# Optimization experiments

Hardware: AMD Instinct MI355X
Metric: run time of the kernel (lower is better)

The kernel has to match this reference:

```python
import jax, jax.numpy as jnp
import numpy as np

# skimage color deconvolution constants: hed_from_rgb = inv(rgb_from_hed)
_RGB_FROM_HED = np.array([[0.65, 0.70, 0.29],
                          [0.07, 0.99, 0.11],
                          [0.27, 0.57, 0.78]], dtype=np.float64)
_HED_FROM_RGB = np.linalg.inv(_RGB_FROM_HED).astype(np.float32)
_LOG_ADJUST = float(np.log(1e-6))  # skimage separate_stains log base


def setup_inputs() -> dict:
    key = jax.random.key(0)
    k1, = jax.random.split(key, 1)
    x = jax.random.uniform(k1, (64, 3, 512, 512), dtype=jnp.float32)  # RGB patches in [0,1]
    gamma = jnp.ones((1,), dtype=jnp.float32)   # InstanceNorm2d affine weight
    beta = jnp.zeros((1,), dtype=jnp.float32)   # InstanceNorm2d affine bias
    return {"x": x, "gamma": gamma, "beta": beta}


def reference(x, gamma, beta):
    h_weights = jnp.asarray(_HED_FROM_RGB[:, 0])  # only H (hematoxylin) column needed, shape (3,)

    # --- skimage.color.separate_stains, batched (replaces per-sample CPU loop) ---
    rgb = jnp.clip(x, 0.0, 1.0)                  # torch.clamp(t, 0, 1)
    rgb = jnp.maximum(rgb, 1e-6)                 # avoid log(0)
    od = jnp.log(rgb) / _LOG_ADJUST              # optical density, (B,3,H,W)
    h = jnp.einsum('bchw,c->bhw', od, h_weights) # stain matrix multiply, H channel only
    h = jnp.maximum(h, 0.0)[:, None, :, :]       # (B,1,H,W), skimage clips stains at 0

    # --- FFT magnitude spectrum ---
    fft = jnp.fft.fft2(h, norm='forward')        # complex64, scaled by 1/(H*W)
    fft = jnp.fft.fftshift(fft, axes=(-2, -1))
    mag = jnp.abs(fft)

    # --- _normalize_log_fft: log1p then per-image min-max ---
    log_mag = jnp.log1p(mag)
    mn = jnp.min(log_mag, axis=(-2, -1), keepdims=True)
    mx = jnp.max(log_mag, axis=(-2, -1), keepdims=True)
    rng = mx - mn
    safe_rng = jnp.where(rng > 0, rng, 1.0)
    normed = jnp.where(rng > 0, (log_mag - mn) / safe_rng, 0.0)

    # --- nn.InstanceNorm2d(1, affine=True), eps=1e-5 ---
    mu = jnp.mean(normed, axis=(-2, -1), keepdims=True)
    var = jnp.var(normed, axis=(-2, -1), keepdims=True)
    out = (normed - mu) * jax.lax.rsqrt(var + 1e-5)
    return out * gamma[None, :, None, None] + beta[None, :, None, None]
```

## Files before the change

### kernel.cpp

```cpp
#include <hip/hip_runtime.h>
#include <hip/hip_fp16.h>
#include <math.h>


#define PI_F 3.14159265358979323846f
#define FROW 264
#define LMSTR 264
#define LVMAX 1.6f
#define QE (65535.0f / LVMAX)
#define QD (LVMAX / 65535.0f)
#define XSTR 568

__device__ __forceinline__ int MU(int p) {
    return ((p >> 6) * 72) + (p & 56) + ((p & 7) ^ ((p >> 3) & 7));
}
__device__ __forceinline__ int odrev(int k) {
    return ((k & 7) << 6) | (k & 56) | (k >> 6);
}

__device__ __forceinline__ float2 cadd(float2 a, float2 b) { return make_float2(a.x + b.x, a.y + b.y); }
__device__ __forceinline__ float2 csub(float2 a, float2 b) { return make_float2(a.x - b.x, a.y - b.y); }
__device__ __forceinline__ float2 cmul(float2 a, float2 w) {
    return make_float2(a.x * w.x - a.y * w.y, a.x * w.y + a.y * w.x);
}

__device__ __forceinline__ void dft8(float2 v[8]) {
    const float s = 0.70710678118654752f;
    float2 a0 = cadd(v[0], v[4]), b0 = csub(v[0], v[4]);
    float2 a1 = cadd(v[1], v[5]), b1 = csub(v[1], v[5]);
    float2 a2 = cadd(v[2], v[6]), b2 = csub(v[2], v[6]);
    float2 a3 = cadd(v[3], v[7]), b3 = csub(v[3], v[7]);
    b1 = make_float2(s * (b1.x + b1.y), s * (b1.y - b1.x));
    b2 = make_float2(b2.y, -b2.x);
    b3 = make_float2(s * (b3.y - b3.x), -s * (b3.x + b3.y));
    float2 c0 = cadd(a0, a2), c1 = cadd(a1, a3);
    float2 d0 = csub(a0, a2), d1 = csub(a1, a3);
    d1 = make_float2(d1.y, -d1.x);
    v[0] = cadd(c0, c1); v[4] = csub(c0, c1);
    v[2] = cadd(d0, d1); v[6] = csub(d0, d1);
    float2 e0 = cadd(b0, b2), e1 = cadd(b1, b3);
    float2 f0 = csub(b0, b2), f1 = csub(b1, b3);
    f1 = make_float2(f1.y, -f1.x);
    v[1] = cadd(e0, e1); v[5] = csub(e0, e1);
    v[3] = cadd(f0, f1); v[7] = csub(f0, f1);
}

__device__ __forceinline__ void fft512_reg(float2* Xw, const float2* TW, int lane) {
    float2 v[8];
    #pragma unroll
    for (int m = 0; m < 8; ++m) v[m] = Xw[MU(lane + (m << 6))];
    dft8(v);
    #pragma unroll
    for (int m = 1; m < 8; ++m) v[m] = cmul(v[m], TW[(lane * m) & 511]);
    #pragma unroll
    for (int m = 0; m < 8; ++m) Xw[MU((m << 6) + lane)] = v[m];
    __builtin_amdgcn_wave_barrier();
    const int b = lane >> 3, t = lane & 7;
    const int base2 = (b << 6) + t;
    #pragma unroll
    for (int m = 0; m < 8; ++m) v[m] = Xw[MU(base2 + (m << 3))];
    dft8(v);
    #pragma unroll
    for (int m = 1; m < 8; ++m) v[m] = cmul(v[m], TW[(t * m) << 3]);
    #pragma unroll
    for (int m = 0; m < 8; ++m) Xw[MU(base2 + (m << 3))] = v[m];
    __builtin_amdgcn_wave_barrier();
    const int base3 = (b << 6) + (t << 3);
    #pragma unroll
    for (int j = 0; j < 8; ++j) v[j] = Xw[MU(base3 + j)];
    dft8(v);
    #pragma unroll
    for (int sidx = 0; sidx < 8; ++sidx) Xw[MU(base3 + sidx)] = v[sidx];
    __builtin_amdgcn_wave_barrier();
}

__device__ __forceinline__ void hstore(float2* Xw, int c,
                                       float r0v, float g0v, float b0v,
                                       float r1v, float g1v, float b1v,
                                       float w0, float w1, float w2) {
    r0v = fminf(fmaxf(r0v, 1e-6f), 1.0f);
    g0v = fminf(fmaxf(g0v, 1e-6f), 1.0f);
    b0v = fminf(fmaxf(b0v, 1e-6f), 1.0f);
    r1v = fminf(fmaxf(r1v, 1e-6f), 1.0f);
    g1v = fminf(fmaxf(g1v, 1e-6f), 1.0f);
    b1v = fminf(fmaxf(b1v, 1e-6f), 1.0f);
    float h0 = fmaxf(w0 * __log2f(r0v) + w1 * __log2f(g0v) + w2 * __log2f(b0v), 0.0f);
    float h1 = fmaxf(w0 * __log2f(r1v) + w1 * __log2f(g1v) + w2 * __log2f(b1v), 0.0f);
    Xw[MU(c)] = make_float2(h0, h1);
}

__global__ __launch_bounds__(256) void k_rowfft(const float* __restrict__ x,
                                                __half2* __restrict__ Fh,
                                                float w0, float w1, float w2) {
    const int b = blockIdx.x >> 6;
    const int p = blockIdx.x & 63;
    __shared__ float2 X[4 * XSTR];
    __shared__ float2 TW[512];
    const int tid = threadIdx.x;
    const int w = tid >> 6, lane = tid & 63;
    #pragma unroll
    for (int t = 0; t < 8; ++t) {
        int idx = lane + (t << 6);
        float sn, cs;
        __sincosf(-PI_F * (float)idx * (1.0f / 256.0f), &sn, &cs);
        TW[idx] = make_float2(cs, sn);
    }
    float2* Xw = X + w * XSTR;
    const float* xb = x + (size_t)b * 786432;
    const int r0 = (p << 3) + (w << 1);

    #pragma unroll
    for (int q = 0; q < 2; ++q) {
        const int cb = (q << 8) + (lane << 2);
        float4 R0 = *(const float4*)(xb +          (r0 << 9) + cb);
        float4 G0 = *(const float4*)(xb + 262144 + (r0 << 9) + cb);
        float4 B0 = *(const float4*)(xb + 524288 + (r0 << 9) + cb);
        float4 R1 = *(const float4*)(xb +          ((r0 + 1) << 9) + cb);
        float4 G1 = *(const float4*)(xb + 262144 + ((r0 + 1) << 9) + cb);
        float4 B1 = *(const float4*)(xb + 524288 + ((r0 + 1) << 9) + cb);
        hstore(Xw, cb + 0, R0.x, G0.x, B0.x, R1.x, G1.x, B1.x, w0, w1, w2);
        hstore(Xw, cb + 1, R0.y, G0.y, B0.y, R1.y, G1.y, B1.y, w0, w1, w2);
        hstore(Xw, cb + 2, R0.z, G0.z, B0.z, R1.z, G1.z, B1.z, w0, w1, w2);
        hstore(Xw, cb + 3, R0.w, G0.w, B0.w, R1.w, G1.w, B1.w, w0, w1, w2);
    }
    __builtin_amdgcn_wave_barrier();

    fft512_reg(Xw, TW, lane);

    __half2* Fb = Fh + (size_t)b * (512 * FROW);
    #pragma unroll
    for (int t = 0; t < 4; ++t) {
        int k = lane + (t << 6);
        int m = (512 - k) & 511;
        float2 zk = Xw[MU(odrev(k))];
        float2 zm = Xw[MU(odrev(m))];
        Fb[r0 * FROW + k]       = __floats2half2_rn(0.5f * (zk.x + zm.x),  0.5f * (zk.y - zm.y));
        Fb[(r0 + 1) * FROW + k] = __floats2half2_rn(0.5f * (zk.y + zm.y), -0.5f * (zk.x - zm.x));
    }
    if (lane == 0) {
        float2 z = Xw[MU(odrev(256))];
        Fb[r0 * FROW + 256]       = __floats2half2_rn(z.x, 0.0f);
        Fb[(r0 + 1) * FROW + 256] = __floats2half2_rn(z.y, 0.0f);
    }
}

__global__ __launch_bounds__(512) void k_colfft(const __half2* __restrict__ Fh,
                                                unsigned short* __restrict__ lmu,
                                                float4* __restrict__ partials) {
    const int b = blockIdx.x / 17;
    const int g = blockIdx.x % 17;
    __shared__ float2 X[8 * XSTR];
    __shared__ float2 TW[512];
    __shared__ float4 wred[8];
    const int tid = threadIdx.x;
    const int w = tid >> 6, lane = tid & 63;
    {
        float sn, cs;
        __sincosf(-PI_F * (float)tid * (1.0f / 256.0f), &sn, &cs);
        TW[tid] = make_float2(cs, sn);
    }
    const __half2* Fb = Fh + (size_t)b * (512 * FROW);
    unsigned short* lm_b = lmu + (size_t)b * (512 * LMSTR);
    float mn = 1e30f, mx = -1e30f, s1 = 0.0f, s2 = 0.0f;

    for (int pass = 0; pass < 2; ++pass) {
        const int u0 = (g << 4) + (pass << 3);
        __syncthreads();
        for (int i = tid; i < 4096; i += 512) {
            int y = i >> 3, c = i & 7;
            int u = u0 + c;
            float2 v = (u <= 256) ? __half22float2(Fb[y * FROW + u])
                                  : make_float2(0.0f, 0.0f);
            X[c * XSTR + MU(y)] = v;
        }
        __syncthreads();
        fft512_reg(X + w * XSTR, TW, lane);
        __syncthreads();
        for (int i = tid; i < 4096; i += 512) {
            int k = i >> 3, c = i & 7;
            int u = u0 + c;
            if (u > 256) continue;
            float2 v = X[c * XSTR + MU(odrev(k))];
            float lv = __log2f(1.0f + sqrtf(v.x * v.x + v.y * v.y));
            int ro = (k + 256) & 511;
            unsigned q = (unsigned)__float2uint_rn(fminf(lv, LVMAX) * QE);
            lm_b[ro * LMSTR + u] = (unsigned short)q;
            mn = fminf(mn, lv);
            mx = fmaxf(mx, lv);
            if (u == 0 || u == 256) { s1 += lv;        s2 += lv * lv; }
            else                    { s1 += 2.0f * lv; s2 += 2.0f * lv * lv; }
        }
    }

    #pragma unroll
    for (int off = 32; off > 0; off >>= 1) {
        mn = fminf(mn, __shfl_down(mn, off, 64));
        mx = fmaxf(mx, __shfl_down(mx, off, 64));
        s1 += __shfl_down(s1, off, 64);
        s2 += __shfl_down(s2, off, 64);
    }
    if (lane == 0) wred[w] = make_float4(mn, mx, s1, s2);
    __syncthreads();
    if (tid == 0) {
        float4 r = wred[0];
        #pragma unroll
        for (int wv = 1; wv < 8; ++wv) {
            float4 q2 = wred[wv];
            r.x = fminf(r.x, q2.x);
            r.y = fmaxf(r.y, q2.y);
            r.z += q2.z;
            r.w += q2.w;
        }
        partials[blockIdx.x] = r;
    }
}

__global__ __launch_bounds__(256) void k_norm(const unsigned short* __restrict__ lmu,
                                              float* __restrict__ out,
                                              const float4* __restrict__ partials,
                                              const float* __restrict__ gamma,
                                              const float* __restrict__ beta) {
    const int p = blockIdx.x & 255;
    const int b = blockIdx.x >> 8;
    float A, B;
    {
        float mn = 1e30f, mx = -1e30f, s1 = 0.0f, s2 = 0.0f;
        #pragma unroll 1
        for (int j = 0; j < 17; ++j) {
            float4 r = partials[b * 17 + j];
            mn = fminf(mn, r.x);
            mx = fmaxf(mx, r.y);
            s1 += r.z;
            s2 += r.w;
        }
        const float N = 262144.0f;
        float mean = s1 / N;
        float var = fmaxf(s2 / N - mean * mean, 0.0f);
        float rng = mx - mn;
        float gm = gamma[0], bt = beta[0];
        if (rng > 0.0f) {
            float inv = 1.0f / rng;
            float varn = var * inv * inv;
            float sc = 1.0f / sqrtf(varn + 1e-5f);
            A = gm * sc * inv;
            B = bt - mean * A;
        } else {
            A = 0.0f;
            B = bt;
        }
    }
    const int rA = p;
    const int rB = (p == 0) ? 256 : 512 - p;
    const unsigned short* lb = lmu + (size_t)b * (512 * LMSTR);
    float* ob = out + ((size_t)b << 18);
    const int tid = threadIdx.x;
    #pragma unroll
    for (int hh = 0; hh < 2; ++hh) {
        const int r = hh ? rB : rA;
        const int rm = (512 - r) & 511;
        const unsigned short* Ld = lb + (size_t)r * LMSTR;
        const unsigned short* Lm = lb + (size_t)rm * LMSTR;
        float lvd = (float)Ld[tid] * QD;
        ob[(r << 9) + 256 + tid] = A * lvd + B;
        float lvm = (tid == 0) ? ((float)Ld[256] * QD)
                               : ((float)Lm[256 - tid] * QD);
        ob[(r << 9) + tid] = A * lvm + B;
    }
}

extern "C" void kernel_launch(void* const* d_in, const int* in_sizes, int n_in,
                              void* d_out, int out_size, void* d_ws, size_t ws_size,
                              hipStream_t stream) {
    const float* x     = (const float*)d_in[0];
    const float* gamma = (const float*)d_in[1];
    const float* beta  = (const float*)d_in[2];
    float* out = (float*)d_out;

    __half2* Fh = (__half2*)d_ws;
    unsigned short* lmu = (unsigned short*)((char*)d_ws + ((size_t)40 << 20));
    float4* partials = (float4*)((char*)d_ws + ((size_t)60 << 20));

    const double M00=0.65, M01=0.70, M02=0.29;
    const double M10=0.07, M11=0.99, M12=0.11;
    const double M20=0.27, M21=0.57, M22=0.78;
    const double det = M00*(M11*M22 - M12*M21)
                     - M01*(M10*M22 - M12*M20)
                     + M02*(M10*M21 - M11*M20);
    const float hw0 = (float)( (M11*M22 - M12*M21) / det);
    const float hw1 = (float)(-(M10*M22 - M12*M20) / det);
    const float hw2 = (float)( (M10*M21 - M11*M20) / det);
    const float invLA2 = (float)(log(2.0) / log(1e-6));
    const float sN = 1.0f / (512.0f * 512.0f);
    const float w0 = hw0 * invLA2 * sN;
    const float w1 = hw1 * invLA2 * sN;
    const float w2 = hw2 * invLA2 * sN;

    k_rowfft<<<64 * 64, 256, 0, stream>>>(x, Fh, w0, w1, w2);
    k_colfft<<<64 * 17, 512, 0, stream>>>(Fh, lmu, partials);
    k_norm<<<64 * 256, 256, 0, stream>>>(lmu, out, partials, gamma, beta);
}
```

Baseline: 123.1 us.

## Rebalance column FFT into 16 blocks per image and split norm coefficients into separate kernel

The column FFT kernel now uses 256-thread blocks with four columns per pass and 16 blocks per image. Block 0 handles the Nyquist column in an extra single-wave pass, replacing the earlier 17th mostly-idle block that zero-padded. A new small kernel computes the per-image affine coefficients once, so each normalization block no longer reduces 17 partials. The normalization kernel also handles four row pairs per block. The changes add a kernel launch and load imbalance on block 0, and the twiddle table is filled with a negated second half.

```diff
diff --git a/kernel.cpp b/kernel.cpp
--- a/kernel.cpp
+++ b/kernel.cpp
@@ -9,7 +9,7 @@
 #define LVMAX 1.6f
 #define QE (65535.0f / LVMAX)
 #define QD (LVMAX / 65535.0f)
-#define XSTR 568
+#define XSTR 570
 
 __device__ __forceinline__ int MU(int p) {
     return ((p >> 6) * 72) + (p & 56) + ((p & 7) ^ ((p >> 3) & 7));
@@ -144,51 +144,70 @@
     }
 }
 
-__global__ __launch_bounds__(512) void k_colfft(const __half2* __restrict__ Fh,
-                                                unsigned short* __restrict__ lmu,
-                                                float4* __restrict__ partials) {
-    const int b = blockIdx.x / 17;
-    const int g = blockIdx.x % 17;
-    __shared__ float2 X[8 * XSTR];
+__global__ __launch_bounds__(256, 4) void k_colfft(const __half2* __restrict__ Fh,
+                                                   unsigned short* __restrict__ lmu,
+                                                   float4* __restrict__ partials) {
+    const int b = blockIdx.x >> 4;
+    const int g = blockIdx.x & 15;
+    __shared__ float2 X[4 * XSTR];
     __shared__ float2 TW[512];
-    __shared__ float4 wred[8];
+    __shared__ float4 wred[4];
     const int tid = threadIdx.x;
     const int w = tid >> 6, lane = tid & 63;
     {
         float sn, cs;
         __sincosf(-PI_F * (float)tid * (1.0f / 256.0f), &sn, &cs);
         TW[tid] = make_float2(cs, sn);
+        TW[tid + 256] = make_float2(-cs, -sn);
     }
     const __half2* Fb = Fh + (size_t)b * (512 * FROW);
     unsigned short* lm_b = lmu + (size_t)b * (512 * LMSTR);
     float mn = 1e30f, mx = -1e30f, s1 = 0.0f, s2 = 0.0f;
-
-    for (int pass = 0; pass < 2; ++pass) {
-        const int u0 = (g << 4) + (pass << 3);
+    const int npass = (g == 0) ? 5 : 4;
+
+    for (int pass = 0; pass < npass; ++pass) {
         __syncthreads();
-        for (int i = tid; i < 4096; i += 512) {
-            int y = i >> 3, c = i & 7;
-            int u = u0 + c;
-            float2 v = (u <= 256) ? __half22float2(Fb[y * FROW + u])
-                                  : make_float2(0.0f, 0.0f);
-            X[c * XSTR + MU(y)] = v;
+        if (pass < 4) {
+            const int u0 = (g << 4) + (pass << 2);
+            for (int i = tid; i < 2048; i += 256) {
+                int y = i >> 2, c = i & 3;
+                float2 v = __half22float2(Fb[y * FROW + u0 + c]);
+                X[c * XSTR + MU(y)] = v;
+            }
+        } else {
+            for (int i = tid; i < 512; i += 256)
+                X[MU(i)] = __half22float2(Fb[i * FROW + 256]);
         }
         __syncthreads();
-        fft512_reg(X + w * XSTR, TW, lane);
+        if (pass < 4 || w == 0)
+            fft512_reg(X + (pass < 4 ? w * XSTR : 0), TW, lane);
         __syncthreads();
-        for (int i = tid; i < 4096; i += 512) {
-            int k = i >> 3, c = i & 7;
-            int u = u0 + c;
-            if (u > 256) continue;
-            float2 v = X[c * XSTR + MU(odrev(k))];
-            float lv = __log2f(1.0f + sqrtf(v.x * v.x + v.y * v.y));
-            int ro = (k + 256) & 511;
-            unsigned q = (unsigned)__float2uint_rn(fminf(lv, LVMAX) * QE);
-            lm_b[ro * LMSTR + u] = (unsigned short)q;
-            mn = fminf(mn, lv);
-            mx = fmaxf(mx, lv);
-            if (u == 0 || u == 256) { s1 += lv;        s2 += lv * lv; }
-            else                    { s1 += 2.0f * lv; s2 += 2.0f * lv * lv; }
+        if (pass < 4) {
+            const int u0 = (g << 4) + (pass << 2);
+            for (int i = tid; i < 2048; i += 256) {
+                int k = i >> 2, c = i & 3;
+                int u = u0 + c;
+                float2 v = X[c * XSTR + MU(odrev(k))];
+                float lv = __log2f(1.0f + sqrtf(v.x * v.x + v.y * v.y));
+                int ro = (k + 256) & 511;
+                unsigned q = (unsigned)__float2uint_rn(fminf(lv, LVMAX) * QE);
+                lm_b[ro * LMSTR + u] = (unsigned short)q;
+                mn = fminf(mn, lv);
+                mx = fmaxf(mx, lv);
+                if (u == 0) { s1 += lv;        s2 += lv * lv; }
+                else        { s1 += 2.0f * lv; s2 += 2.0f * lv * lv; }
+            }
+        } else {
+            for (int i = tid; i < 512; i += 256) {
+                float2 v = X[MU(odrev(i))];
+                float lv = __log2f(1.0f + sqrtf(v.x * v.x + v.y * v.y));
+                int ro = (i + 256) & 511;
+                unsigned q = (unsigned)__float2uint_rn(fminf(lv, LVMAX) * QE);
+                lm_b[ro * LMSTR + 256] = (unsigned short)q;
+                mn = fminf(mn, lv);
+                mx = fmaxf(mx, lv);
+                s1 += lv; s2 += lv * lv;
+            }
         }
     }
 
@@ -204,7 +223,7 @@
     if (tid == 0) {
         float4 r = wred[0];
         #pragma unroll
-        for (int wv = 1; wv < 8; ++wv) {
+        for (int wv = 1; wv < 4; ++wv) {
             float4 q2 = wred[wv];
             r.x = fminf(r.x, q2.x);
             r.y = fmaxf(r.y, q2.y);
@@ -215,56 +234,71 @@
     }
 }
 
-__global__ __launch_bounds__(256) void k_norm(const unsigned short* __restrict__ lmu,
-                                              float* __restrict__ out,
-                                              const float4* __restrict__ partials,
+__global__ __launch_bounds__(64) void k_coeff(const float4* __restrict__ partials,
                                               const float* __restrict__ gamma,
-                                              const float* __restrict__ beta) {
-    const int p = blockIdx.x & 255;
-    const int b = blockIdx.x >> 8;
-    float A, B;
-    {
-        float mn = 1e30f, mx = -1e30f, s1 = 0.0f, s2 = 0.0f;
-        #pragma unroll 1
-        for (int j = 0; j < 17; ++j) {
-            float4 r = partials[b * 17 + j];
-            mn = fminf(mn, r.x);
-            mx = fmaxf(mx, r.y);
-            s1 += r.z;
-            s2 += r.w;
-        }
+                                              const float* __restrict__ beta,
+                                              float2* __restrict__ coeff) {
+    const int b = blockIdx.x;
+    float mn = 1e30f, mx = -1e30f, s1 = 0.0f, s2 = 0.0f;
+    if (threadIdx.x < 16) {
+        float4 r = partials[(b << 4) + threadIdx.x];
+        mn = r.x; mx = r.y; s1 = r.z; s2 = r.w;
+    }
+    #pragma unroll
+    for (int off = 32; off > 0; off >>= 1) {
+        mn = fminf(mn, __shfl_down(mn, off, 64));
+        mx = fmaxf(mx, __shfl_down(mx, off, 64));
+        s1 += __shfl_down(s1, off, 64);
+        s2 += __shfl_down(s2, off, 64);
+    }
+    if (threadIdx.x == 0) {
         const float N = 262144.0f;
         float mean = s1 / N;
         float var = fmaxf(s2 / N - mean * mean, 0.0f);
         float rng = mx - mn;
-        float gm = gamma[0], bt = beta[0];
+        float g = gamma[0], bt = beta[0];
+        float A, B;
         if (rng > 0.0f) {
             float inv = 1.0f / rng;
             float varn = var * inv * inv;
             float sc = 1.0f / sqrtf(varn + 1e-5f);
-            A = gm * sc * inv;
+            A = g * sc * inv;
             B = bt - mean * A;
         } else {
             A = 0.0f;
             B = bt;
         }
-    }
-    const int rA = p;
-    const int rB = (p == 0) ? 256 : 512 - p;
+        coeff[b] = make_float2(A, B);
+    }
+}
+
+__global__ __launch_bounds__(256) void k_norm(const unsigned short* __restrict__ lmu,
+                                              float* __restrict__ out,
+                                              const float2* __restrict__ coeff) {
+    const int j = blockIdx.x & 63;
+    const int b = blockIdx.x >> 6;
+    const float2 ab = coeff[b];
+    const float A = ab.x, B = ab.y;
     const unsigned short* lb = lmu + (size_t)b * (512 * LMSTR);
     float* ob = out + ((size_t)b << 18);
     const int tid = threadIdx.x;
     #pragma unroll
-    for (int hh = 0; hh < 2; ++hh) {
-        const int r = hh ? rB : rA;
-        const int rm = (512 - r) & 511;
-        const unsigned short* Ld = lb + (size_t)r * LMSTR;
-        const unsigned short* Lm = lb + (size_t)rm * LMSTR;
-        float lvd = (float)Ld[tid] * QD;
-        ob[(r << 9) + 256 + tid] = A * lvd + B;
-        float lvm = (tid == 0) ? ((float)Ld[256] * QD)
-                               : ((float)Lm[256 - tid] * QD);
-        ob[(r << 9) + tid] = A * lvm + B;
+    for (int pp = 0; pp < 4; ++pp) {
+        const int p = (j << 2) + pp;
+        const int rA = p;
+        const int rB = (p == 0) ? 256 : 512 - p;
+        #pragma unroll
+        for (int hh = 0; hh < 2; ++hh) {
+            const int r = hh ? rB : rA;
+            const int rm = (512 - r) & 511;
+            const unsigned short* Ld = lb + (size_t)r * LMSTR;
+            const unsigned short* Lm = lb + (size_t)rm * LMSTR;
+            float lvd = (float)Ld[tid] * QD;
+            ob[(r << 9) + 256 + tid] = A * lvd + B;
+            float lvm = (tid == 0) ? ((float)Ld[256] * QD)
+                                   : ((float)Lm[256 - tid] * QD);
+            ob[(r << 9) + tid] = A * lvm + B;
+        }
     }
 }
 
@@ -279,6 +313,7 @@
     __half2* Fh = (__half2*)d_ws;
     unsigned short* lmu = (unsigned short*)((char*)d_ws + ((size_t)40 << 20));
     float4* partials = (float4*)((char*)d_ws + ((size_t)60 << 20));
+    float2* coeff    = (float2*)((char*)d_ws + ((size_t)60 << 20) + 1024 * sizeof(float4));
 
     const double M00=0.65, M01=0.70, M02=0.29;
     const double M10=0.07, M11=0.99, M12=0.11;
@@ -296,6 +331,7 @@
     const float w2 = hw2 * invLA2 * sN;
 
     k_rowfft<<<64 * 64, 256, 0, stream>>>(x, Fh, w0, w1, w2);
-    k_colfft<<<64 * 17, 512, 0, stream>>>(Fh, lmu, partials);
-    k_norm<<<64 * 256, 256, 0, stream>>>(lmu, out, partials, gamma, beta);
-}
+    k_colfft<<<64 * 16, 256, 0, stream>>>(Fh, lmu, partials);
+    k_coeff<<<64, 64, 0, stream>>>(partials, gamma, beta, coeff);
+    k_norm<<<64 * 64, 256, 0, stream>>>(lmu, out, coeff);
+}
```

Result: slower. 132.1 us (+7.3%).

## Pack DC and Nyquist columns into one complex FFT, add coefficient kernel

Applied to the files above, without the earlier changes.

The column FFT stage previously used 17 groups of 16 columns per image, with the 17th group mostly empty, to cover columns 0..256. The real-valued columns 0 and 256 are now packed as the real and imaginary parts of one complex column and separated after the FFT by conjugate symmetry, so 16 groups cover everything and the wasted 17th block per image is gone. The per-image normalisation coefficients are also computed once in a small separate kernel instead of being recomputed from the partials by every k_norm block, at the cost of one extra launch.

```diff
diff --git a/kernel.cpp b/kernel.cpp
--- a/kernel.cpp
+++ b/kernel.cpp
@@ -147,8 +147,8 @@
 __global__ __launch_bounds__(512) void k_colfft(const __half2* __restrict__ Fh,
                                                 unsigned short* __restrict__ lmu,
                                                 float4* __restrict__ partials) {
-    const int b = blockIdx.x / 17;
-    const int g = blockIdx.x % 17;
+    const int b = blockIdx.x >> 4;
+    const int g = blockIdx.x & 15;
     __shared__ float2 X[8 * XSTR];
     __shared__ float2 TW[512];
     __shared__ float4 wred[8];
@@ -165,12 +165,18 @@
 
     for (int pass = 0; pass < 2; ++pass) {
         const int u0 = (g << 4) + (pass << 3);
+        const bool packpass = (g == 0 && pass == 0);
         __syncthreads();
         for (int i = tid; i < 4096; i += 512) {
             int y = i >> 3, c = i & 7;
-            int u = u0 + c;
-            float2 v = (u <= 256) ? __half22float2(Fb[y * FROW + u])
-                                  : make_float2(0.0f, 0.0f);
+            float2 v;
+            if (packpass && c == 0) {
+                float2 f0   = __half22float2(Fb[y * FROW]);
+                float2 f256 = __half22float2(Fb[y * FROW + 256]);
+                v = make_float2(f0.x, f256.x);
+            } else {
+                v = __half22float2(Fb[y * FROW + u0 + c]);
+            }
             X[c * XSTR + MU(y)] = v;
         }
         __syncthreads();
@@ -178,17 +184,34 @@
         __syncthreads();
         for (int i = tid; i < 4096; i += 512) {
             int k = i >> 3, c = i & 7;
-            int u = u0 + c;
-            if (u > 256) continue;
-            float2 v = X[c * XSTR + MU(odrev(k))];
-            float lv = __log2f(1.0f + sqrtf(v.x * v.x + v.y * v.y));
             int ro = (k + 256) & 511;
-            unsigned q = (unsigned)__float2uint_rn(fminf(lv, LVMAX) * QE);
-            lm_b[ro * LMSTR + u] = (unsigned short)q;
-            mn = fminf(mn, lv);
-            mx = fmaxf(mx, lv);
-            if (u == 0 || u == 256) { s1 += lv;        s2 += lv * lv; }
-            else                    { s1 += 2.0f * lv; s2 += 2.0f * lv * lv; }
+            if (packpass && c == 0) {
+                int m = (512 - k) & 511;
+                float2 zk = X[MU(odrev(k))];
+                float2 zm = X[MU(odrev(m))];
+                float2 c0   = make_float2(0.5f * (zk.x + zm.x),  0.5f * (zk.y - zm.y));
+                float2 c256 = make_float2(0.5f * (zk.y + zm.y), -0.5f * (zk.x - zm.x));
+                float lv0   = __log2f(1.0f + sqrtf(c0.x * c0.x + c0.y * c0.y));
+                float lv256 = __log2f(1.0f + sqrtf(c256.x * c256.x + c256.y * c256.y));
+                unsigned q0 = (unsigned)__float2uint_rn(fminf(lv0,   LVMAX) * QE);
+                unsigned q6 = (unsigned)__float2uint_rn(fminf(lv256, LVMAX) * QE);
+                lm_b[ro * LMSTR]       = (unsigned short)q0;
+                lm_b[ro * LMSTR + 256] = (unsigned short)q6;
+                mn = fminf(mn, fminf(lv0, lv256));
+                mx = fmaxf(mx, fmaxf(lv0, lv256));
+                s1 += lv0 + lv256;
+                s2 += lv0 * lv0 + lv256 * lv256;
+            } else {
+                int u = u0 + c;
+                float2 v = X[c * XSTR + MU(odrev(k))];
+                float lv = __log2f(1.0f + sqrtf(v.x * v.x + v.y * v.y));
+                unsigned q = (unsigned)__float2uint_rn(fminf(lv, LVMAX) * QE);
+                lm_b[ro * LMSTR + u] = (unsigned short)q;
+                mn = fminf(mn, lv);
+                mx = fmaxf(mx, lv);
+                s1 += 2.0f * lv;
+                s2 += 2.0f * lv * lv;
+            }
         }
     }
 
@@ -215,40 +238,51 @@
     }
 }
 
-__global__ __launch_bounds__(256) void k_norm(const unsigned short* __restrict__ lmu,
-                                              float* __restrict__ out,
-                                              const float4* __restrict__ partials,
+__global__ __launch_bounds__(64) void k_coeff(const float4* __restrict__ partials,
                                               const float* __restrict__ gamma,
-                                              const float* __restrict__ beta) {
-    const int p = blockIdx.x & 255;
-    const int b = blockIdx.x >> 8;
-    float A, B;
-    {
-        float mn = 1e30f, mx = -1e30f, s1 = 0.0f, s2 = 0.0f;
-        #pragma unroll 1
-        for (int j = 0; j < 17; ++j) {
-            float4 r = partials[b * 17 + j];
-            mn = fminf(mn, r.x);
-            mx = fmaxf(mx, r.y);
-            s1 += r.z;
-            s2 += r.w;
-        }
+                                              const float* __restrict__ beta,
+                                              float2* __restrict__ coeff) {
+    const int b = blockIdx.x;
+    float mn = 1e30f, mx = -1e30f, s1 = 0.0f, s2 = 0.0f;
+    if (threadIdx.x < 16) {
+        float4 r = partials[(b << 4) + threadIdx.x];
+        mn = r.x; mx = r.y; s1 = r.z; s2 = r.w;
+    }
+    #pragma unroll
+    for (int off = 32; off > 0; off >>= 1) {
+        mn = fminf(mn, __shfl_down(mn, off, 64));
+        mx = fmaxf(mx, __shfl_down(mx, off, 64));
+        s1 += __shfl_down(s1, off, 64);
+        s2 += __shfl_down(s2, off, 64);
+    }
+    if (threadIdx.x == 0) {
         const float N = 262144.0f;
         float mean = s1 / N;
         float var = fmaxf(s2 / N - mean * mean, 0.0f);
         float rng = mx - mn;
-        float gm = gamma[0], bt = beta[0];
+        float g = gamma[0], bt = beta[0];
+        float A, B;
         if (rng > 0.0f) {
             float inv = 1.0f / rng;
             float varn = var * inv * inv;
             float sc = 1.0f / sqrtf(varn + 1e-5f);
-            A = gm * sc * inv;
+            A = g * sc * inv;
             B = bt - mean * A;
         } else {
             A = 0.0f;
             B = bt;
         }
-    }
+        coeff[b] = make_float2(A, B);
+    }
+}
+
+__global__ __launch_bounds__(256) void k_norm(const unsigned short* __restrict__ lmu,
+                                              float* __restrict__ out,
+                                              const float2* __restrict__ coeff) {
+    const int p = blockIdx.x & 255;
+    const int b = blockIdx.x >> 8;
+    const float2 ab = coeff[b];
+    const float A = ab.x, B = ab.y;
     const int rA = p;
     const int rB = (p == 0) ? 256 : 512 - p;
     const unsigned short* lb = lmu + (size_t)b * (512 * LMSTR);
@@ -279,6 +313,7 @@
     __half2* Fh = (__half2*)d_ws;
     unsigned short* lmu = (unsigned short*)((char*)d_ws + ((size_t)40 << 20));
     float4* partials = (float4*)((char*)d_ws + ((size_t)60 << 20));
+    float2* coeff    = (float2*)((char*)d_ws + ((size_t)60 << 20) + 1024 * sizeof(float4));
 
     const double M00=0.65, M01=0.70, M02=0.29;
     const double M10=0.07, M11=0.99, M12=0.11;
@@ -296,6 +331,7 @@
     const float w2 = hw2 * invLA2 * sN;
 
     k_rowfft<<<64 * 64, 256, 0, stream>>>(x, Fh, w0, w1, w2);
-    k_colfft<<<64 * 17, 512, 0, stream>>>(Fh, lmu, partials);
-    k_norm<<<64 * 256, 256, 0, stream>>>(lmu, out, partials, gamma, beta);
-}
+    k_colfft<<<64 * 16, 512, 0, stream>>>(Fh, lmu, partials);
+    k_coeff<<<64, 64, 0, stream>>>(partials, gamma, beta, coeff);
+    k_norm<<<64 * 256, 256, 0, stream>>>(lmu, out, coeff);
+}
```

Result: faster. 118.3 us (-3.9%).
